# Kernel tuning notes

Measured on AMD Instinct MI355X. Metric: run time of the kernel, lower is better.

Reference implementation:

```python
import jax, jax.numpy as jnp
import numpy as np

NUM_EXPERTS = 8
TOP_K = 2
N_EMBD = 1024
BLOCK_SIZE = 128
# d_ffn = round_up(4*n_embd // top_k, block_size)
D_FFN = ((4 * N_EMBD // TOP_K + BLOCK_SIZE - 1) // BLOCK_SIZE) * BLOCK_SIZE  # 2048
TOTAL_WIDTH = NUM_EXPERTS * D_FFN  # 16384


def setup_inputs() -> dict:
    key = jax.random.key(0)
    k1, k2, k3, k4 = jax.random.split(key, 4)
    x = jax.random.normal(k1, (4, 2048, N_EMBD), dtype=jnp.float32)
    # router: nn.Linear(n_embd, num_experts, bias=False) -> weight [E, n_embd]
    w_router = jax.random.normal(k2, (NUM_EXPERTS, N_EMBD), dtype=jnp.float32) * 0.02
    w1 = jax.random.normal(k3, (N_EMBD, TOTAL_WIDTH), dtype=jnp.float32) * 0.02
    w2 = jax.random.normal(k4, (TOTAL_WIDTH, N_EMBD), dtype=jnp.float32) * 0.02
    return {"x": x, "w_router": w_router, "w1": w1, "w2": w2}


def reference(x, w_router, w1, w2):
    B, S, N = x.shape
    T = B * S
    x_flat = x.reshape(T, N)

    # Router
    router_logits = x_flat @ w_router.T                       # [T, E]
    router_probs = jax.nn.softmax(router_logits.astype(jnp.float32), axis=-1)
    expert_weights, selected_experts = jax.lax.top_k(router_probs, TOP_K)  # [T, K]
    # norm_topk_prob=True
    expert_weights = expert_weights / expert_weights.sum(axis=-1, keepdims=True)
    expert_weights = expert_weights.astype(x.dtype)

    # Expert computation. The original does a sort/gather + block-sparse grouped
    # GEMM; math-equivalently, each token's output is
    #   sum_k w_k * gelu(x @ W1_e) @ W2_e  for e = selected_experts[:, k].
    # Loop over the small fixed expert set, masking per-token combine weights.
    out = jnp.zeros((T, N), dtype=x.dtype)
    for e in range(NUM_EXPERTS):
        off = e * D_FFN
        # combine weight for expert e per token (0 if not routed there)
        w_e = jnp.where(selected_experts == e, expert_weights, 0.0).sum(axis=-1)  # [T]
        h = jax.nn.gelu(x_flat @ w1[:, off:off + D_FFN], approximate=False)       # [T, D_FFN]
        out = out + w_e[:, None] * (h @ w2[off:off + D_FFN, :])

    output = out.reshape(B, S, N)

    # Aux losses
    router_z_loss = jnp.mean(jax.nn.logsumexp(router_logits, axis=-1) ** 2)
    p_i = router_probs.mean(axis=0).astype(x.dtype)            # [E]
    flat_sel = selected_experts.reshape(-1)
    f_i = jnp.zeros((NUM_EXPERTS,), dtype=x.dtype).at[flat_sel].add(1.0 / flat_sel.shape[0])
    load_balance_loss = NUM_EXPERTS * (f_i @ p_i)

    return output, router_z_loss, load_balance_loss, f_i
```

## Files before the change

kernel.cpp:

```cpp
#include <hip/hip_runtime.h>
#include <hip/hip_bf16.h>
#include <math.h>

#define T_TOK 8192
#define NE 1024
#define N_EXP 8
#define DFFN 2048
#define TW 16384
#define P_TOT 16384

#define BMT 128
#define BNT 128
#define BK9 32

typedef __attribute__((ext_vector_type(8))) short bf16x8;
typedef __attribute__((ext_vector_type(4))) float f32x4;

#define GLOAD_LDS16(g, l) __builtin_amdgcn_global_load_lds( \
    (const __attribute__((address_space(1))) void*)(g), \
    (__attribute__((address_space(3))) void*)(l), 16, 0, 0)

static __device__ __forceinline__ unsigned short f2bf(float f) {
    __hip_bfloat16 b = __float2bfloat16(f);
    return *(unsigned short*)&b;
}

static __device__ __forceinline__ float gelu_fast(float v) {
    float u2 = v * (1.5957691216f + 0.0713548162f * v * v);
    return v / (1.f + __expf(-u2));
}

__global__ __launch_bounds__(256) void router_kernel(
    const float* __restrict__ x, const float* __restrict__ wr,
    int* __restrict__ sel_idx, float* __restrict__ sel_wt,
    float* __restrict__ z_part, float* __restrict__ p_part,
    unsigned short* __restrict__ xb)
{
    __shared__ float wrs[N_EXP * NE];
    __shared__ float zred[32];
    __shared__ float pred[32][8];
    int tid = threadIdx.x;
    for (int i = tid; i < N_EXP * NE / 4; i += 256)
        ((float4*)wrs)[i] = ((const float4*)wr)[i];
    __syncthreads();

    int slot = tid >> 3, oct = tid & 7;
    int t = blockIdx.x * 32 + slot;
    float lg[N_EXP];
#pragma unroll
    for (int e = 0; e < N_EXP; e++) lg[e] = 0.f;

    const float4* x4 = (const float4*)(x + (size_t)t * NE) + oct * 32;
    for (int n4 = 0; n4 < 32; n4++) {
        float4 xv = x4[n4];
        ushort4 o;
        o.x = f2bf(xv.x); o.y = f2bf(xv.y); o.z = f2bf(xv.z); o.w = f2bf(xv.w);
        *(ushort4*)&xb[(size_t)t * NE + oct * 128 + n4 * 4] = o;
#pragma unroll
        for (int e = 0; e < N_EXP; e++) {
            const float* w = &wrs[e * NE + oct * 128 + n4 * 4];
            lg[e] += xv.x * w[0] + xv.y * w[1] + xv.z * w[2] + xv.w * w[3];
        }
    }
#pragma unroll
    for (int d = 1; d < 8; d <<= 1)
#pragma unroll
        for (int e = 0; e < N_EXP; e++) lg[e] += __shfl_xor(lg[e], d);

    float m = lg[0];
#pragma unroll
    for (int e = 1; e < N_EXP; e++) m = fmaxf(m, lg[e]);
    float p[N_EXP], s = 0.f;
#pragma unroll
    for (int e = 0; e < N_EXP; e++) { p[e] = expf(lg[e] - m); s += p[e]; }
    float inv = 1.f / s;
#pragma unroll
    for (int e = 0; e < N_EXP; e++) p[e] *= inv;
    float lse = m + logf(s);

    int e0 = 0;
#pragma unroll
    for (int e = 1; e < N_EXP; e++) if (p[e] > p[e0]) e0 = e;
    int e1 = (e0 == 0) ? 1 : 0;
#pragma unroll
    for (int e = 0; e < N_EXP; e++) if (e != e0 && p[e] > p[e1]) e1 = e;

    if (oct == 0) {
        float wn = 1.f / (p[e0] + p[e1]);
        sel_idx[t * 2 + 0] = e0;
        sel_idx[t * 2 + 1] = e1;
        sel_wt[t * 2 + 0] = p[e0] * wn;
        sel_wt[t * 2 + 1] = p[e1] * wn;
        zred[slot] = lse * lse;
#pragma unroll
        for (int e = 0; e < N_EXP; e++) pred[slot][e] = p[e];
    }
    __syncthreads();
    if (tid == 0) {
        float zs = 0.f;
        for (int i = 0; i < 32; i++) zs += zred[i];
        z_part[blockIdx.x] = zs;
        for (int e = 0; e < N_EXP; e++) {
            float ps = 0.f;
            for (int i = 0; i < 32; i++) ps += pred[i][e];
            p_part[blockIdx.x * N_EXP + e] = ps;
        }
    }
}

__global__ __launch_bounds__(256) void finalize_router(
    const int* __restrict__ sel_idx,
    const float* __restrict__ z_part, const float* __restrict__ p_part,
    int* __restrict__ cnt, int* __restrict__ off, int* __restrict__ cursor,
    float* __restrict__ out)
{
    __shared__ int redc[256];
    __shared__ float redf[256];
    __shared__ int cnts[N_EXP];
    __shared__ float psum[N_EXP];
    __shared__ float zsum;
    int tid = threadIdx.x;

    int c[N_EXP];
#pragma unroll
    for (int e = 0; e < N_EXP; e++) c[e] = 0;
    for (int i = tid; i < P_TOT; i += 256) c[sel_idx[i]]++;
#pragma unroll
    for (int e = 0; e < N_EXP; e++) {
        redc[tid] = c[e];
        __syncthreads();
        for (int st = 128; st > 0; st >>= 1) {
            if (tid < st) redc[tid] += redc[tid + st];
            __syncthreads();
        }
        if (tid == 0) cnts[e] = redc[0];
        __syncthreads();
    }

    redf[tid] = z_part[tid];
    __syncthreads();
    for (int st = 128; st > 0; st >>= 1) {
        if (tid < st) redf[tid] += redf[tid + st];
        __syncthreads();
    }
    if (tid == 0) zsum = redf[0];
    __syncthreads();

#pragma unroll
    for (int e = 0; e < N_EXP; e++) {
        redf[tid] = p_part[tid * N_EXP + e];
        __syncthreads();
        for (int st = 128; st > 0; st >>= 1) {
            if (tid < st) redf[tid] += redf[tid + st];
            __syncthreads();
        }
        if (tid == 0) psum[e] = redf[0];
        __syncthreads();
    }

    if (tid == 0) {
        int o = 0;
        for (int e = 0; e < N_EXP; e++) {
            cnt[e] = cnts[e];
            off[e] = o;
            o += cnts[e];
            cursor[e] = 0;
        }
        off[N_EXP] = o;
        float lb = 0.f;
        float* tail = out + (size_t)T_TOK * NE;
        for (int e = 0; e < N_EXP; e++) {
            float fi = (float)cnts[e] / (float)P_TOT;
            float pi = psum[e] / (float)T_TOK;
            lb += fi * pi;
            tail[2 + e] = fi;
        }
        tail[0] = zsum / (float)T_TOK;
        tail[1] = 8.f * lb;
    }
}

__global__ __launch_bounds__(256) void scatter_kernel(
    const int* __restrict__ sel_idx, const int* __restrict__ off,
    int* __restrict__ cursor, int* __restrict__ token_list)
{
    int i = blockIdx.x * 256 + threadIdx.x;
    if (i < P_TOT) {
        int e = sel_idx[i];
        int pos = atomicAdd(&cursor[e], 1);
        token_list[off[e] + pos] = i;
    }
}

__global__ __launch_bounds__(256) void transpose_both_kernel(
    const float* __restrict__ w1, unsigned short* __restrict__ w1t,
    const float* __restrict__ w2, unsigned short* __restrict__ w2t)
{
    __shared__ float tile[64][65];
    const float* src;
    unsigned short* dst;
    int R, C, rb, cb;
    int bid = blockIdx.x;
    if (bid < 4096) {
        src = w1; dst = w1t; R = NE; C = TW;
        cb = (bid & 255) * 64; rb = (bid >> 8) * 64;
    } else {
        int b2 = bid - 4096;
        src = w2; dst = w2t; R = TW; C = NE;
        cb = (b2 & 15) * 64; rb = (b2 >> 4) * 64;
    }
    int tid = threadIdx.x;
#pragma unroll
    for (int p = 0; p < 4; p++) {
        int idx = p * 256 + tid;
        int r = idx >> 4, c4 = (idx & 15) << 2;
        float4 v = *(const float4*)&src[(size_t)(rb + r) * C + cb + c4];
        tile[r][c4 + 0] = v.x; tile[r][c4 + 1] = v.y;
        tile[r][c4 + 2] = v.z; tile[r][c4 + 3] = v.w;
    }
    __syncthreads();
#pragma unroll
    for (int p = 0; p < 4; p++) {
        int idx = p * 256 + tid;
        int c = idx >> 4, r4 = (idx & 15) << 2;
        ushort4 o;
        o.x = f2bf(tile[r4 + 0][c]); o.y = f2bf(tile[r4 + 1][c]);
        o.z = f2bf(tile[r4 + 2][c]); o.w = f2bf(tile[r4 + 3][c]);
        *(ushort4*)&dst[(size_t)(cb + c) * R + rb + r4] = o;
    }
}

#define STG(buf, kb) do {                                                 \
    GLOAD_LDS16(asrc0 + (kb), &As[buf][wid * 1024]);                      \
    GLOAD_LDS16(asrc1 + (kb), &As[buf][wid * 1024 + 512]);                \
    GLOAD_LDS16(bsrc0 + (kb), &Bs[buf][wid * 1024]);                      \
    GLOAD_LDS16(bsrc1 + (kb), &Bs[buf][wid * 1024 + 512]);                \
} while (0)

#define GEMM_LOOP(NKT)                                                    \
    STG(0, 0);                                                            \
    __syncthreads();                                                      \
    for (int t = 0; t < (NKT); t++) {                                     \
        int cur = t & 1;                                                  \
        if (t + 1 < (NKT)) STG(cur ^ 1, (t + 1) * BK9);                   \
        bf16x8 af[4], bfr[4];                                             \
        _Pragma("unroll")                                                 \
        for (int m = 0; m < 4; m++)                                       \
            af[m] = *(const bf16x8*)&As[cur][(wm * 64 + m * 16 + rr) * BK9 + kqa * 8]; \
        _Pragma("unroll")                                                 \
        for (int n = 0; n < 4; n++)                                       \
            bfr[n] = *(const bf16x8*)&Bs[cur][(wn * 64 + n * 16 + rr) * BK9 + kqa * 8]; \
        __builtin_amdgcn_s_setprio(1);                                    \
        _Pragma("unroll")                                                 \
        for (int m = 0; m < 4; m++)                                       \
            _Pragma("unroll")                                             \
            for (int n = 0; n < 4; n++)                                   \
                acc[m][n] = __builtin_amdgcn_mfma_f32_16x16x32_bf16(      \
                    af[m], bfr[n], acc[m][n], 0, 0, 0);                   \
        __builtin_amdgcn_s_setprio(0);                                    \
        __syncthreads();                                                  \
    }

__global__ __launch_bounds__(256, 4) void gemm1_mfma(
    const __hip_bfloat16* __restrict__ xb, const __hip_bfloat16* __restrict__ w1t,
    const int* __restrict__ token_list, const float* __restrict__ sel_wt,
    const int* __restrict__ cnt, const int* __restrict__ off,
    __hip_bfloat16* __restrict__ h)
{
    __shared__ __align__(16) __hip_bfloat16 As[2][BMT * BK9];
    __shared__ __align__(16) __hip_bfloat16 Bs[2][BNT * BK9];

    int b = blockIdx.x;
    int e = b & 7;
    int cnt_e = cnt[e];
    int off_e = off[e];
    int njobs = ((cnt_e + BMT - 1) >> 7) * 16;

    int tid = threadIdx.x;
    int wid = tid >> 6, lane = tid & 63;
    int wm = wid >> 1, wn = wid & 1;
    int rr = lane & 15, kq = lane >> 4;
    int kqa = kq ^ ((rr >> 1) & 3);
    int ksw = (lane & 3) ^ ((lane >> 3) & 3);
    int r0 = wid * 32 + (lane >> 2);
    int r1 = r0 + 16;

    for (int j = b >> 3; j < njobs; j += 272) {
        int rowbase = (j >> 4) * BMT;
        int colbase = (j & 15) * BNT;
        int rows_e = cnt_e - rowbase;

        int ent0 = token_list[off_e + rowbase + ((r0 < rows_e) ? r0 : 0)];
        int ent1 = token_list[off_e + rowbase + ((r1 < rows_e) ? r1 : 0)];
        const __hip_bfloat16* asrc0 = xb + (size_t)(ent0 >> 1) * NE + ksw * 8;
        const __hip_bfloat16* asrc1 = xb + (size_t)(ent1 >> 1) * NE + ksw * 8;
        const __hip_bfloat16* bsrc0 = w1t + (size_t)(e * DFFN + colbase + r0) * NE + ksw * 8;
        const __hip_bfloat16* bsrc1 = bsrc0 + (size_t)16 * NE;

        f32x4 acc[4][4] = {};
        GEMM_LOOP(NE / BK9)

        int colg = colbase + wn * 64;
#pragma unroll
        for (int m = 0; m < 4; m++) {
#pragma unroll
            for (int jj = 0; jj < 4; jj++) {
                int r = wm * 64 + m * 16 + kq * 4 + jj;
                if (r < rows_e) {
                    size_t p = (size_t)off_e + rowbase + r;
                    float wgt = sel_wt[token_list[p]];
#pragma unroll
                    for (int n = 0; n < 4; n++) {
                        float g = gelu_fast(acc[m][n][jj]);
                        h[p * DFFN + colg + n * 16 + rr] = __float2bfloat16(wgt * g);
                    }
                }
            }
        }
        __syncthreads();
    }
}

__global__ __launch_bounds__(256, 4) void gemm2_mfma(
    const __hip_bfloat16* __restrict__ h, const __hip_bfloat16* __restrict__ w2t,
    const int* __restrict__ token_list,
    const int* __restrict__ cnt, const int* __restrict__ off,
    float* __restrict__ out)
{
    __shared__ __align__(16) __hip_bfloat16 As[2][BMT * BK9];
    __shared__ __align__(16) __hip_bfloat16 Bs[2][BNT * BK9];

    int b = blockIdx.x;
    int e = b & 7;
    int cnt_e = cnt[e];
    int off_e = off[e];
    int njobs = ((cnt_e + BMT - 1) >> 7) * 8;

    int tid = threadIdx.x;
    int wid = tid >> 6, lane = tid & 63;
    int wm = wid >> 1, wn = wid & 1;
    int rr = lane & 15, kq = lane >> 4;
    int kqa = kq ^ ((rr >> 1) & 3);
    int ksw = (lane & 3) ^ ((lane >> 3) & 3);
    int r0 = wid * 32 + (lane >> 2);
    int r1 = r0 + 16;

    for (int j = b >> 3; j < njobs; j += 136) {
        int rowbase = (j >> 3) * BMT;
        int colbase = (j & 7) * BNT;
        int rows_e = cnt_e - rowbase;

        int pr0 = off_e + rowbase + ((r0 < rows_e) ? r0 : 0);
        int pr1 = off_e + rowbase + ((r1 < rows_e) ? r1 : 0);
        const __hip_bfloat16* asrc0 = h + (size_t)pr0 * DFFN + ksw * 8;
        const __hip_bfloat16* asrc1 = h + (size_t)pr1 * DFFN + ksw * 8;
        const __hip_bfloat16* bsrc0 = w2t + (size_t)(colbase + r0) * TW + e * DFFN + ksw * 8;
        const __hip_bfloat16* bsrc1 = bsrc0 + (size_t)16 * TW;

        f32x4 acc[4][4] = {};
        GEMM_LOOP(DFFN / BK9)

        int colg = colbase + wn * 64;
#pragma unroll
        for (int m = 0; m < 4; m++) {
#pragma unroll
            for (int jj = 0; jj < 4; jj++) {
                int r = wm * 64 + m * 16 + kq * 4 + jj;
                if (r < rows_e) {
                    size_t p = (size_t)off_e + rowbase + r;
                    int tok = token_list[p] >> 1;
#pragma unroll
                    for (int n = 0; n < 4; n++)
                        atomicAdd(&out[(size_t)tok * NE + colg + n * 16 + rr],
                                  acc[m][n][jj]);
                }
            }
        }
        __syncthreads();
    }
}

extern "C" void kernel_launch(void* const* d_in, const int* in_sizes, int n_in,
                              void* d_out, int out_size, void* d_ws, size_t ws_size,
                              hipStream_t stream)
{
    const float* x  = (const float*)d_in[0];
    const float* wr = (const float*)d_in[1];
    const float* w1 = (const float*)d_in[2];
    const float* w2 = (const float*)d_in[3];
    float* out = (float*)d_out;

    char* ws = (char*)d_ws;
    size_t o = 0;
    __hip_bfloat16* h   = (__hip_bfloat16*)(ws + o); o += (size_t)P_TOT * DFFN * 2;
    __hip_bfloat16* xb  = (__hip_bfloat16*)(ws + o); o += (size_t)T_TOK * NE * 2;
    __hip_bfloat16* w1t = (__hip_bfloat16*)(ws + o); o += (size_t)NE * TW * 2;
    __hip_bfloat16* w2t = (__hip_bfloat16*)(ws + o); o += (size_t)TW * NE * 2;
    int*   sel_idx    = (int*)(ws + o);   o += P_TOT * 4;
    float* sel_wt     = (float*)(ws + o); o += P_TOT * 4;
    int*   token_list = (int*)(ws + o);   o += P_TOT * 4;
    int*   cnt        = (int*)(ws + o);   o += 64;
    int*   off        = (int*)(ws + o);   o += 64;
    int*   cursor     = (int*)(ws + o);   o += 64;
    float* z_part     = (float*)(ws + o); o += 256 * 4;
    float* p_part     = (float*)(ws + o); o += 256 * N_EXP * 4;

    hipMemsetAsync(d_out, 0, (size_t)out_size * sizeof(float), stream);

    router_kernel<<<256, 256, 0, stream>>>(x, wr, sel_idx, sel_wt, z_part, p_part,
                                           (unsigned short*)xb);
    transpose_both_kernel<<<8192, 256, 0, stream>>>(
        w1, (unsigned short*)w1t, w2, (unsigned short*)w2t);
    finalize_router<<<1, 256, 0, stream>>>(sel_idx, z_part, p_part, cnt, off, cursor,
                                           out);
    scatter_kernel<<<64, 256, 0, stream>>>(sel_idx, off, cursor, token_list);

    gemm1_mfma<<<2176, 256, 0, stream>>>(
        xb, w1t, token_list, sel_wt, cnt, off, h);
    gemm2_mfma<<<1088, 256, 0, stream>>>(
        h, w2t, token_list, cnt, off, out);
}
```

Baseline: 448.6 us.

## Use 256x256x64 tiles with 8-wave blocks and interleaved load/MFMA schedule

Replaces the 128x128x32 four-wave grouped GEMM tiles with 256x256x64 tiles computed by eight waves, using 128KB of dynamic LDS split into double-buffered halves. The K loop is broken into four quadrant phases that interleave async global-to-LDS loads with MFMA batches, controlled by explicit barriers, waitcnt and sched_barrier. The launch grids shrink to 512 and 256 persistent blocks. The aim is higher arithmetic intensity per LDS load and better overlap of memory with math. The cost is one block per CU, more padding waste on the partial row tiles of each expert, and heavy register use from 32 accumulators per thread.

```diff
diff --git a/kernel.cpp b/kernel.cpp
--- a/kernel.cpp
+++ b/kernel.cpp
@@ -8,10 +8,6 @@
 #define DFFN 2048
 #define TW 16384
 #define P_TOT 16384
-
-#define BMT 128
-#define BNT 128
-#define BK9 32
 
 typedef __attribute__((ext_vector_type(8))) short bf16x8;
 typedef __attribute__((ext_vector_type(4))) float f32x4;
@@ -230,89 +226,146 @@
     }
 }
 
-#define STG(buf, kb) do {                                                 \
-    GLOAD_LDS16(asrc0 + (kb), &As[buf][wid * 1024]);                      \
-    GLOAD_LDS16(asrc1 + (kb), &As[buf][wid * 1024 + 512]);                \
-    GLOAD_LDS16(bsrc0 + (kb), &Bs[buf][wid * 1024]);                      \
-    GLOAD_LDS16(bsrc1 + (kb), &Bs[buf][wid * 1024 + 512]);                \
+#define BAR   __builtin_amdgcn_s_barrier()
+#define SB0   __builtin_amdgcn_sched_barrier(0)
+#define LGKM0 asm volatile("s_waitcnt lgkmcnt(0)" ::: "memory")
+#define VMC(n) asm volatile("s_waitcnt vmcnt(" #n ")" ::: "memory")
+
+#define STG_A(hh, koff, nb) do {                                          \
+    GLOAD_LDS16(aS[hh][0] + (koff), Asm + (nb) + (hh)*8192 + wid*1024 + lane*8); \
+    GLOAD_LDS16(aS[hh][1] + (koff), Asm + (nb) + (hh)*8192 + wid*1024 + 512 + lane*8); \
 } while (0)
-
-#define GEMM_LOOP(NKT)                                                    \
-    STG(0, 0);                                                            \
-    __syncthreads();                                                      \
+#define STG_B(hh, koff, nb) do {                                          \
+    GLOAD_LDS16(bS[hh][0] + (koff), Bsm + (nb) + (hh)*8192 + wid*1024 + lane*8); \
+    GLOAD_LDS16(bS[hh][1] + (koff), Bsm + (nb) + (hh)*8192 + wid*1024 + 512 + lane*8); \
+} while (0)
+
+#define RD_A(mh, cb) do {                                                 \
+    _Pragma("unroll")                                                     \
+    for (int m4 = 0; m4 < 4; m4++) {                                      \
+        int ro = (wm*128 + ((mh)*4 + m4)*16 + rr) * 64;                   \
+        av[m4*2 + 0] = *(const bf16x8*)&Asm[(cb) + ro + ks0];             \
+        av[m4*2 + 1] = *(const bf16x8*)&Asm[(cb) + ro + ks1];             \
+    } } while (0)
+#define RD_B(nh, cb) do {                                                 \
+    _Pragma("unroll")                                                     \
+    for (int n2 = 0; n2 < 2; n2++) {                                      \
+        int ro = (wn*64 + ((nh)*2 + n2)*16 + rr) * 64;                    \
+        bv[(nh)*4 + n2*2 + 0] = *(const bf16x8*)&Bsm[(cb) + ro + ks0];    \
+        bv[(nh)*4 + n2*2 + 1] = *(const bf16x8*)&Bsm[(cb) + ro + ks1];    \
+    } } while (0)
+
+#define MFMA_Q(mh, nh) do {                                               \
+    __builtin_amdgcn_s_setprio(1);                                        \
+    _Pragma("unroll")                                                     \
+    for (int m4 = 0; m4 < 4; m4++)                                        \
+        _Pragma("unroll")                                                 \
+        for (int n2 = 0; n2 < 2; n2++) {                                  \
+            acc[(mh)*4+m4][(nh)*2+n2] = __builtin_amdgcn_mfma_f32_16x16x32_bf16( \
+                av[m4*2+0], bv[(nh)*4+n2*2+0], acc[(mh)*4+m4][(nh)*2+n2], 0, 0, 0); \
+            acc[(mh)*4+m4][(nh)*2+n2] = __builtin_amdgcn_mfma_f32_16x16x32_bf16( \
+                av[m4*2+1], bv[(nh)*4+n2*2+1], acc[(mh)*4+m4][(nh)*2+n2], 0, 0, 0); \
+        }                                                                 \
+    __builtin_amdgcn_s_setprio(0);                                        \
+} while (0)
+
+#define GEMM_CORE(NKT)                                                    \
+    bf16x8 av[8], bv[8];                                                  \
+    STG_A(0, 0, 0); STG_A(1, 0, 0); STG_B(0, 0, 0); STG_B(1, 0, 0);       \
+    VMC(0); BAR;                                                          \
     for (int t = 0; t < (NKT); t++) {                                     \
-        int cur = t & 1;                                                  \
-        if (t + 1 < (NKT)) STG(cur ^ 1, (t + 1) * BK9);                   \
-        bf16x8 af[4], bfr[4];                                             \
-        _Pragma("unroll")                                                 \
-        for (int m = 0; m < 4; m++)                                       \
-            af[m] = *(const bf16x8*)&As[cur][(wm * 64 + m * 16 + rr) * BK9 + kqa * 8]; \
-        _Pragma("unroll")                                                 \
-        for (int n = 0; n < 4; n++)                                       \
-            bfr[n] = *(const bf16x8*)&Bs[cur][(wn * 64 + n * 16 + rr) * BK9 + kqa * 8]; \
-        __builtin_amdgcn_s_setprio(1);                                    \
-        _Pragma("unroll")                                                 \
-        for (int m = 0; m < 4; m++)                                       \
-            _Pragma("unroll")                                             \
-            for (int n = 0; n < 4; n++)                                   \
-                acc[m][n] = __builtin_amdgcn_mfma_f32_16x16x32_bf16(      \
-                    af[m], bfr[n], acc[m][n], 0, 0, 0);                   \
-        __builtin_amdgcn_s_setprio(0);                                    \
-        __syncthreads();                                                  \
-    }
-
-__global__ __launch_bounds__(256, 4) void gemm1_mfma(
+        int cb = (t & 1) << 14;                                           \
+        int nb = cb ^ 16384;                                              \
+        int koff = (t + 1) * 64;                                          \
+        bool pf = (t + 1 < (NKT));                                        \
+                                                             \
+        if (pf) { STG_A(0, koff, nb); SB0; VMC(2); } else { VMC(0); }     \
+        BAR;                                                              \
+        RD_A(0, cb); RD_B(0, cb);                                         \
+        LGKM0; SB0;                                                       \
+        MFMA_Q(0, 0);                                                     \
+        SB0; BAR;                                                         \
+                                                             \
+        RD_B(1, cb);                                                      \
+        if (pf) STG_A(1, koff, nb);                                       \
+        BAR; LGKM0; SB0;                                                  \
+        MFMA_Q(0, 1);                                                     \
+        SB0; BAR;                                                         \
+                                                             \
+        RD_A(1, cb);                                                      \
+        if (pf) STG_B(0, koff, nb);                                       \
+        BAR; LGKM0; SB0;                                                  \
+        MFMA_Q(1, 0);                                                     \
+        SB0; BAR;                                                         \
+                                                             \
+        if (pf) STG_B(1, koff, nb);                                       \
+        BAR;                                                              \
+        MFMA_Q(1, 1);                                                     \
+        SB0; BAR;                                                         \
+    }
+
+#define GEMM_SETUP16()                                                    \
+    int tid = threadIdx.x;                                                \
+    int wid = tid >> 6, lane = tid & 63;                                  \
+    int wm = wid >> 2, wn = wid & 3;                                      \
+    int rr = lane & 15, kq = lane >> 4;                                   \
+    int rs = rr & 7;                                                      \
+    int ks0 = (kq ^ rs) * 8;                                              \
+    int ks1 = ((4 + kq) ^ rs) * 8;                                        \
+    int ksw8 = (lane & 7) ^ (lane >> 3);                                  \
+    int lrow = lane >> 3;
+
+__global__ __launch_bounds__(512) void gemm1_mfma(
     const __hip_bfloat16* __restrict__ xb, const __hip_bfloat16* __restrict__ w1t,
     const int* __restrict__ token_list, const float* __restrict__ sel_wt,
     const int* __restrict__ cnt, const int* __restrict__ off,
-    __hip_bfloat16* __restrict__ h)
-{
-    __shared__ __align__(16) __hip_bfloat16 As[2][BMT * BK9];
-    __shared__ __align__(16) __hip_bfloat16 Bs[2][BNT * BK9];
+    __hip_bfloat16* __restrict__ hout)
+{
+    extern __shared__ __align__(16) __hip_bfloat16 smem[];
+    __hip_bfloat16* Asm = smem;
+    __hip_bfloat16* Bsm = smem + 32768;
 
     int b = blockIdx.x;
     int e = b & 7;
-    int cnt_e = cnt[e];
-    int off_e = off[e];
-    int njobs = ((cnt_e + BMT - 1) >> 7) * 16;
-
-    int tid = threadIdx.x;
-    int wid = tid >> 6, lane = tid & 63;
-    int wm = wid >> 1, wn = wid & 1;
-    int rr = lane & 15, kq = lane >> 4;
-    int kqa = kq ^ ((rr >> 1) & 3);
-    int ksw = (lane & 3) ^ ((lane >> 3) & 3);
-    int r0 = wid * 32 + (lane >> 2);
-    int r1 = r0 + 16;
-
-    for (int j = b >> 3; j < njobs; j += 272) {
-        int rowbase = (j >> 4) * BMT;
-        int colbase = (j & 15) * BNT;
+    int cnt_e = cnt[e], off_e = off[e];
+    int nrt = (cnt_e + 255) >> 8;
+    int njobs = nrt * 8;
+
+    GEMM_SETUP16()
+
+    for (int j = b >> 3; j < njobs; j += 64) {
+        int rowbase = (j >> 3) * 256;
+        int colb = (j & 7) * 256;
         int rows_e = cnt_e - rowbase;
 
-        int ent0 = token_list[off_e + rowbase + ((r0 < rows_e) ? r0 : 0)];
-        int ent1 = token_list[off_e + rowbase + ((r1 < rows_e) ? r1 : 0)];
-        const __hip_bfloat16* asrc0 = xb + (size_t)(ent0 >> 1) * NE + ksw * 8;
-        const __hip_bfloat16* asrc1 = xb + (size_t)(ent1 >> 1) * NE + ksw * 8;
-        const __hip_bfloat16* bsrc0 = w1t + (size_t)(e * DFFN + colbase + r0) * NE + ksw * 8;
-        const __hip_bfloat16* bsrc1 = bsrc0 + (size_t)16 * NE;
-
-        f32x4 acc[4][4] = {};
-        GEMM_LOOP(NE / BK9)
-
-        int colg = colbase + wn * 64;
-#pragma unroll
-        for (int m = 0; m < 4; m++) {
-#pragma unroll
-            for (int jj = 0; jj < 4; jj++) {
-                int r = wm * 64 + m * 16 + kq * 4 + jj;
+        const __hip_bfloat16* aS[2][2];
+        const __hip_bfloat16* bS[2][2];
+#pragma unroll
+        for (int hh = 0; hh < 2; hh++)
+#pragma unroll
+            for (int jj = 0; jj < 2; jj++) {
+                int r = hh * 128 + wid * 16 + jj * 8 + lrow;
+                int ent = token_list[off_e + rowbase + ((r < rows_e) ? r : 0)];
+                aS[hh][jj] = xb + (size_t)(ent >> 1) * NE + ksw8 * 8;
+                bS[hh][jj] = w1t + (size_t)(e * DFFN + colb + r) * NE + ksw8 * 8;
+            }
+
+        f32x4 acc[8][4] = {};
+        GEMM_CORE(NE / 64)
+
+        int colg = colb + wn * 64;
+#pragma unroll
+        for (int m = 0; m < 8; m++) {
+#pragma unroll
+            for (int q4 = 0; q4 < 4; q4++) {
+                int r = wm * 128 + m * 16 + kq * 4 + q4;
                 if (r < rows_e) {
                     size_t p = (size_t)off_e + rowbase + r;
                     float wgt = sel_wt[token_list[p]];
 #pragma unroll
                     for (int n = 0; n < 4; n++) {
-                        float g = gelu_fast(acc[m][n][jj]);
-                        h[p * DFFN + colg + n * 16 + rr] = __float2bfloat16(wgt * g);
+                        float g = gelu_fast(acc[m][n][q4]);
+                        hout[p * DFFN + colg + n * 16 + rr] = __float2bfloat16(wgt * g);
                     }
                 }
             }
@@ -321,58 +374,57 @@
     }
 }
 
-__global__ __launch_bounds__(256, 4) void gemm2_mfma(
-    const __hip_bfloat16* __restrict__ h, const __hip_bfloat16* __restrict__ w2t,
+__global__ __launch_bounds__(512) void gemm2_mfma(
+    const __hip_bfloat16* __restrict__ hsrc, const __hip_bfloat16* __restrict__ w2t,
     const int* __restrict__ token_list,
     const int* __restrict__ cnt, const int* __restrict__ off,
     float* __restrict__ out)
 {
-    __shared__ __align__(16) __hip_bfloat16 As[2][BMT * BK9];
-    __shared__ __align__(16) __hip_bfloat16 Bs[2][BNT * BK9];
+    extern __shared__ __align__(16) __hip_bfloat16 smem[];
+    __hip_bfloat16* Asm = smem;
+    __hip_bfloat16* Bsm = smem + 32768;
 
     int b = blockIdx.x;
     int e = b & 7;
-    int cnt_e = cnt[e];
-    int off_e = off[e];
-    int njobs = ((cnt_e + BMT - 1) >> 7) * 8;
-
-    int tid = threadIdx.x;
-    int wid = tid >> 6, lane = tid & 63;
-    int wm = wid >> 1, wn = wid & 1;
-    int rr = lane & 15, kq = lane >> 4;
-    int kqa = kq ^ ((rr >> 1) & 3);
-    int ksw = (lane & 3) ^ ((lane >> 3) & 3);
-    int r0 = wid * 32 + (lane >> 2);
-    int r1 = r0 + 16;
-
-    for (int j = b >> 3; j < njobs; j += 136) {
-        int rowbase = (j >> 3) * BMT;
-        int colbase = (j & 7) * BNT;
+    int cnt_e = cnt[e], off_e = off[e];
+    int nrt = (cnt_e + 255) >> 8;
+    int njobs = nrt * 4;
+
+    GEMM_SETUP16()
+
+    for (int j = b >> 3; j < njobs; j += 32) {
+        int rowbase = (j >> 2) * 256;
+        int colb = (j & 3) * 256;
         int rows_e = cnt_e - rowbase;
 
-        int pr0 = off_e + rowbase + ((r0 < rows_e) ? r0 : 0);
-        int pr1 = off_e + rowbase + ((r1 < rows_e) ? r1 : 0);
-        const __hip_bfloat16* asrc0 = h + (size_t)pr0 * DFFN + ksw * 8;
-        const __hip_bfloat16* asrc1 = h + (size_t)pr1 * DFFN + ksw * 8;
-        const __hip_bfloat16* bsrc0 = w2t + (size_t)(colbase + r0) * TW + e * DFFN + ksw * 8;
-        const __hip_bfloat16* bsrc1 = bsrc0 + (size_t)16 * TW;
-
-        f32x4 acc[4][4] = {};
-        GEMM_LOOP(DFFN / BK9)
-
-        int colg = colbase + wn * 64;
-#pragma unroll
-        for (int m = 0; m < 4; m++) {
-#pragma unroll
-            for (int jj = 0; jj < 4; jj++) {
-                int r = wm * 64 + m * 16 + kq * 4 + jj;
+        const __hip_bfloat16* aS[2][2];
+        const __hip_bfloat16* bS[2][2];
+#pragma unroll
+        for (int hh = 0; hh < 2; hh++)
+#pragma unroll
+            for (int jj = 0; jj < 2; jj++) {
+                int r = hh * 128 + wid * 16 + jj * 8 + lrow;
+                int pr = off_e + rowbase + ((r < rows_e) ? r : 0);
+                aS[hh][jj] = hsrc + (size_t)pr * DFFN + ksw8 * 8;
+                bS[hh][jj] = w2t + (size_t)(colb + r) * TW + e * DFFN + ksw8 * 8;
+            }
+
+        f32x4 acc[8][4] = {};
+        GEMM_CORE(DFFN / 64)
+
+        int colg = colb + wn * 64;
+#pragma unroll
+        for (int m = 0; m < 8; m++) {
+#pragma unroll
+            for (int q4 = 0; q4 < 4; q4++) {
+                int r = wm * 128 + m * 16 + kq * 4 + q4;
                 if (r < rows_e) {
                     size_t p = (size_t)off_e + rowbase + r;
                     int tok = token_list[p] >> 1;
 #pragma unroll
                     for (int n = 0; n < 4; n++)
                         atomicAdd(&out[(size_t)tok * NE + colg + n * 16 + rr],
-                                  acc[m][n][jj]);
+                                  acc[m][n][q4]);
                 }
             }
         }
@@ -405,6 +457,11 @@
     float* z_part     = (float*)(ws + o); o += 256 * 4;
     float* p_part     = (float*)(ws + o); o += 256 * N_EXP * 4;
 
+    hipFuncSetAttribute((const void*)gemm1_mfma,
+                        hipFuncAttributeMaxDynamicSharedMemorySize, 131072);
+    hipFuncSetAttribute((const void*)gemm2_mfma,
+                        hipFuncAttributeMaxDynamicSharedMemorySize, 131072);
+
     hipMemsetAsync(d_out, 0, (size_t)out_size * sizeof(float), stream);
 
     router_kernel<<<256, 256, 0, stream>>>(x, wr, sel_idx, sel_wt, z_part, p_part,
@@ -415,8 +472,8 @@
                                            out);
     scatter_kernel<<<64, 256, 0, stream>>>(sel_idx, off, cursor, token_list);
 
-    gemm1_mfma<<<2176, 256, 0, stream>>>(
+    gemm1_mfma<<<512, 512, 131072, stream>>>(
         xb, w1t, token_list, sel_wt, cnt, off, h);
-    gemm2_mfma<<<1088, 256, 0, stream>>>(
+    gemm2_mfma<<<256, 512, 131072, stream>>>(
         h, w2t, token_list, cnt, off, out);
 }
```

Result: slower. 498.1 us (+11.0%).
